# Kernel optimization log

Hardware: AMD Instinct MI355X
Metric: run time of the kernel (lower is better)

The kernel has to match this reference:

```python
import jax, jax.numpy as jnp
import numpy as np

B, T, OBS, ENC, H, A = 32, 512, 256, 1024, 1024, 64
AR_COEF, TAR_COEF = 0.01, 0.01
LN_EPS = 1e-5


def setup_inputs() -> dict:
    key = jax.random.key(0)
    ks = jax.random.split(key, 8)
    s = 0.02  # weight scale to keep activations in a sane range
    # PyTorch LSTM bias init in source: zeros, forget-gate slice [H:2H] = 1.0 (both b_ih and b_hh)
    b_gate = jnp.zeros((4 * H,), jnp.float32).at[H:2 * H].set(1.0)
    return {
        "obs": jax.random.normal(ks[0], (B, T, OBS), jnp.float32),
        "hxs": jnp.zeros((B, H), jnp.float32),
        "cxs": jnp.zeros((B, H), jnp.float32),
        "W1": jax.random.normal(ks[1], (ENC, OBS), jnp.float32) * s,
        "b1": jnp.zeros((ENC,), jnp.float32),
        "W2": jax.random.normal(ks[2], (ENC, ENC), jnp.float32) * s,
        "b2": jnp.zeros((ENC,), jnp.float32),
        "W_ih": jax.random.normal(ks[3], (4 * H, ENC), jnp.float32) * s,
        "W_hh": jax.random.normal(ks[4], (4 * H, H), jnp.float32) * s,
        "b_ih": b_gate,
        "b_hh": b_gate,
        "ln_g": jnp.ones((H,), jnp.float32),
        "ln_b": jnp.zeros((H,), jnp.float32),
        "Wa": jax.random.normal(ks[5], (A, H), jnp.float32) * s,
        "ba": jnp.zeros((A,), jnp.float32),
        "Wc": jax.random.normal(ks[6], (1, H), jnp.float32) * s,
        "bc": jnp.zeros((1,), jnp.float32),
    }


def reference(obs, hxs, cxs, W1, b1, W2, b2, W_ih, W_hh, b_ih, b_hh,
              ln_g, ln_b, Wa, ba, Wc, bc):
    # Encoder: Linear -> SiLU -> Linear -> SiLU
    enc = jax.nn.silu(obs @ W1.T + b1)
    enc = jax.nn.silu(enc @ W2.T + b2)  # (B,T,ENC)

    # LSTM (WeightDrop is identity in eval mode / p=0). Precompute input gates.
    gx = enc @ W_ih.T + (b_ih + b_hh)  # (B,T,4H)

    def step(carry, g_t):
        h, c = carry
        g = g_t + h @ W_hh.T  # (B,4H), PyTorch gate order: i, f, g, o
        i, f, gc, o = jnp.split(g, 4, axis=-1)
        c = jax.nn.sigmoid(f) * c + jax.nn.sigmoid(i) * jnp.tanh(gc)
        h = jax.nn.sigmoid(o) * jnp.tanh(c)
        return (h, c), h

    (h_n, c_n), hs = jax.lax.scan(step, (hxs, cxs), jnp.swapaxes(gx, 0, 1))
    out = jnp.swapaxes(hs, 0, 1)  # (B,T,H)

    # LayerNorm
    mu = out.mean(-1, keepdims=True)
    var = out.var(-1, keepdims=True)
    out = (out - mu) / jnp.sqrt(var + LN_EPS) * ln_g + ln_b

    ar_loss = jnp.mean(out ** 2) * AR_COEF
    tar_loss = jnp.mean((out[:, 1:, :] - out[:, :-1, :]) ** 2) * TAR_COEF

    logits = out @ Wa.T + ba          # (B,T,A)
    values = (out @ Wc.T + bc)[..., 0]  # (B,T)
    return logits, values, h_n, c_n, ar_loss, tar_loss
```

## Files before the change

### kernel.cpp

```cpp
#include <hip/hip_runtime.h>


typedef _Float16 half8 __attribute__((ext_vector_type(8)));
typedef _Float16 half4v __attribute__((ext_vector_type(4)));
typedef float floatx4 __attribute__((ext_vector_type(4)));
typedef unsigned long long ull;

__device__ __forceinline__ float sigmoidf_(float x) { return 1.f / (1.f + __expf(-x)); }

__global__ void k_convert(const float* __restrict__ src, _Float16* __restrict__ dst, int n4) {
  int i = blockIdx.x * blockDim.x + threadIdx.x;
  int stride = gridDim.x * blockDim.x;
  for (; i < n4; i += stride) {
    floatx4 v = *(const floatx4*)(src + (size_t)i * 4);
    half4v h;
    h[0] = (_Float16)v[0]; h[1] = (_Float16)v[1];
    h[2] = (_Float16)v[2]; h[3] = (_Float16)v[3];
    *(half4v*)(dst + (size_t)i * 4) = h;
  }
}

__global__ __launch_bounds__(256) void k_inith(const float* __restrict__ hxs,
                                               _Float16* __restrict__ hstate) {
  int s = blockIdx.x * 256 + threadIdx.x;
  int batch = s >> 9, pair = s & 511;
  union { _Float16 h[2]; unsigned u; } p;
  p.h[0] = (_Float16)hxs[batch * 1024 + pair * 2];
  p.h[1] = (_Float16)hxs[batch * 1024 + pair * 2 + 1];
  *(unsigned*)(hstate + (size_t)batch * 1024 + pair * 2) = p.u;
}

template<int EPI>
__global__ __launch_bounds__(256) void k_gemm(
    const _Float16* __restrict__ A, const _Float16* __restrict__ B,
    _Float16* __restrict__ C, const float* __restrict__ bias0,
    const float* __restrict__ bias1, int M, int N, int K)
{
  __shared__ _Float16 As[128 * 32];
  __shared__ _Float16 Bs[128 * 32];
  const int tid = threadIdx.x;
  const int l = tid & 63;
  const int w = tid >> 6;
  const int wr = w >> 1, wc = w & 1;
  const _Float16* Ab = A + (size_t)blockIdx.x * 128 * K;
  const _Float16* Bb = B + (size_t)blockIdx.y * 128 * K;

  floatx4 acc[4][4];
#pragma unroll
  for (int a = 0; a < 4; ++a)
#pragma unroll
    for (int b = 0; b < 4; ++b) acc[a][b] = (floatx4){0.f, 0.f, 0.f, 0.f};

  const int ci0 = tid, ci1 = tid + 256;
  const int r0 = ci0 >> 2, r1 = ci1 >> 2;
  const int q0 = (ci0 & 3) ^ ((r0 >> 2) & 3);
  const int q1 = (ci1 & 3) ^ ((r1 >> 2) & 3);
  const int lr = l & 15;
  const int ko = l >> 4;
  const int nkt = K >> 5;

  for (int kt = 0; kt < nkt; ++kt) {
    const _Float16* Ak = Ab + kt * 32;
    const _Float16* Bk = Bb + kt * 32;
    uint4 va0 = *(const uint4*)(Ak + (size_t)r0 * K + q0 * 8);
    uint4 va1 = *(const uint4*)(Ak + (size_t)r1 * K + q1 * 8);
    uint4 vb0 = *(const uint4*)(Bk + (size_t)r0 * K + q0 * 8);
    uint4 vb1 = *(const uint4*)(Bk + (size_t)r1 * K + q1 * 8);
    __syncthreads();
    *(uint4*)(As + ci0 * 8) = va0;
    *(uint4*)(As + ci1 * 8) = va1;
    *(uint4*)(Bs + ci0 * 8) = vb0;
    *(uint4*)(Bs + ci1 * 8) = vb1;
    __syncthreads();
    half8 af[4], bf[4];
#pragma unroll
    for (int mr = 0; mr < 4; ++mr) {
      int row = wr * 64 + mr * 16 + lr;
      int cq = ko ^ ((row >> 2) & 3);
      af[mr] = *(const half8*)(As + row * 32 + cq * 8);
    }
#pragma unroll
    for (int nc = 0; nc < 4; ++nc) {
      int col = wc * 64 + nc * 16 + lr;
      int cq = ko ^ ((col >> 2) & 3);
      bf[nc] = *(const half8*)(Bs + col * 32 + cq * 8);
    }
#pragma unroll
    for (int mr = 0; mr < 4; ++mr)
#pragma unroll
      for (int nc = 0; nc < 4; ++nc)
        acc[mr][nc] = __builtin_amdgcn_mfma_f32_16x16x32_f16(af[mr], bf[nc], acc[mr][nc], 0, 0, 0);
  }

  const int lq = l >> 4;
#pragma unroll
  for (int nc = 0; nc < 4; ++nc) {
    int gcol = blockIdx.y * 128 + wc * 64 + nc * 16 + lr;
    float bia = bias0[gcol];
    if (EPI == 1) bia += bias1[gcol];
#pragma unroll
    for (int mr = 0; mr < 4; ++mr) {
      int grow = blockIdx.x * 128 + wr * 64 + mr * 16 + lq * 4;
#pragma unroll
      for (int i = 0; i < 4; ++i) {
        float v = acc[mr][nc][i] + bia;
        if (EPI == 0) v = v * sigmoidf_(v);
        C[(size_t)(grow + i) * N + gcol] = (_Float16)v;
      }
    }
  }
}

__global__ __launch_bounds__(256, 1) void k_scan(
    const _Float16* __restrict__ gx,
    const _Float16* __restrict__ Whh,
    const float* __restrict__ cxs,
    _Float16* __restrict__ hstate,
    int* __restrict__ flags,
    _Float16* __restrict__ outh,
    float* __restrict__ out_hn, float* __restrict__ out_cn)
{
  const int blk = blockIdx.x;
  const int hbase = blk * 16;
  const int tid = threadIdx.x, l = tid & 63, wq = tid >> 6;
  __shared__ float red[4][4][2][4][65];

  const int cc = l & 15, ko = l >> 4;

  half8 bfr[4][8];
#pragma unroll
  for (int q = 0; q < 4; ++q)
#pragma unroll
    for (int kk = 0; kk < 8; ++kk)
      bfr[q][kk] = *(const half8*)(Whh + (size_t)(q * 1024 + hbase + cc) * 1024
                                   + wq * 256 + kk * 32 + ko * 8);

  const int gb = tid >> 3, gc2 = tid & 7;
  float c0 = cxs[gb * 1024 + hbase + gc2 * 2 + 0];
  float c1 = cxs[gb * 1024 + hbase + gc2 * 2 + 1];
  const int gmt = gb >> 4, greg = gb & 3;
  const int lane0 = ((gb & 15) >> 2) * 16 + gc2 * 2;

  unsigned gxv[4];
#pragma unroll
  for (int q = 0; q < 4; ++q)
    gxv[q] = *(const unsigned*)(gx + (size_t)gb * 512 * 4096
                                + q * 1024 + hbase + gc2 * 2);

  for (int t = 0; t < 512; ++t) {
    if (t > 0) {
      if (wq == 0) {
        const int* fp = flags + l * 16;
        int guard = 0;
        while (__hip_atomic_load(fp, __ATOMIC_RELAXED, __HIP_MEMORY_SCOPE_AGENT) < t) {
          if (++guard > (1 << 17)) break;
          __builtin_amdgcn_s_sleep(1);
        }
      }
      __builtin_amdgcn_s_barrier();
      __builtin_amdgcn_sched_barrier(0);
    }

    const _Float16* hcur = hstate + (size_t)(t & 1) * 32768;
    const ull* p0 = (const ull*)(hcur + cc * 1024 + wq * 256 + ko * 8);
    const ull* p1 = (const ull*)(hcur + (16 + cc) * 1024 + wq * 256 + ko * 8);
    ull ld0[16], ld1[16];
#pragma unroll
    for (int kk = 0; kk < 8; ++kk) {
      ld0[kk * 2 + 0] = __hip_atomic_load(p0 + kk * 8 + 0, __ATOMIC_RELAXED, __HIP_MEMORY_SCOPE_AGENT);
      ld0[kk * 2 + 1] = __hip_atomic_load(p0 + kk * 8 + 1, __ATOMIC_RELAXED, __HIP_MEMORY_SCOPE_AGENT);
      ld1[kk * 2 + 0] = __hip_atomic_load(p1 + kk * 8 + 0, __ATOMIC_RELAXED, __HIP_MEMORY_SCOPE_AGENT);
      ld1[kk * 2 + 1] = __hip_atomic_load(p1 + kk * 8 + 1, __ATOMIC_RELAXED, __HIP_MEMORY_SCOPE_AGENT);
    }

    floatx4 acc[4][2];
#pragma unroll
    for (int q = 0; q < 4; ++q) {
      acc[q][0] = (floatx4){0.f, 0.f, 0.f, 0.f};
      acc[q][1] = (floatx4){0.f, 0.f, 0.f, 0.f};
    }
#pragma unroll
    for (int kk = 0; kk < 8; ++kk) {
      union { ull u2[2]; half8 h; } a0, a1;
      a0.u2[0] = ld0[kk * 2 + 0]; a0.u2[1] = ld0[kk * 2 + 1];
      a1.u2[0] = ld1[kk * 2 + 0]; a1.u2[1] = ld1[kk * 2 + 1];
#pragma unroll
      for (int q = 0; q < 4; ++q) {
        acc[q][0] = __builtin_amdgcn_mfma_f32_16x16x32_f16(a0.h, bfr[q][kk], acc[q][0], 0, 0, 0);
        acc[q][1] = __builtin_amdgcn_mfma_f32_16x16x32_f16(a1.h, bfr[q][kk], acc[q][1], 0, 0, 0);
      }
    }
#pragma unroll
    for (int q = 0; q < 4; ++q)
#pragma unroll
      for (int mt = 0; mt < 2; ++mt)
#pragma unroll
        for (int i = 0; i < 4; ++i)
          red[wq][q][mt][i][l] = acc[q][mt][i];
    asm volatile("s_waitcnt lgkmcnt(0)" ::: "memory");
    __builtin_amdgcn_s_barrier();
    __builtin_amdgcn_sched_barrier(0);

    float pre0[4], pre1[4];
#pragma unroll
    for (int q = 0; q < 4; ++q) {
      pre0[q] = red[0][q][gmt][greg][lane0] + red[1][q][gmt][greg][lane0]
              + red[2][q][gmt][greg][lane0] + red[3][q][gmt][greg][lane0];
      pre1[q] = red[0][q][gmt][greg][lane0 + 1] + red[1][q][gmt][greg][lane0 + 1]
              + red[2][q][gmt][greg][lane0 + 1] + red[3][q][gmt][greg][lane0 + 1];
    }
    union { unsigned u; _Float16 h[2]; } g0, g1, g2, g3;
    g0.u = gxv[0]; g1.u = gxv[1]; g2.u = gxv[2]; g3.u = gxv[3];

    float i0 = sigmoidf_(pre0[0] + (float)g0.h[0]);
    float f0 = sigmoidf_(pre0[1] + (float)g1.h[0]);
    float gg0 = tanhf(pre0[2] + (float)g2.h[0]);
    float o0 = sigmoidf_(pre0[3] + (float)g3.h[0]);
    c0 = f0 * c0 + i0 * gg0;
    float h0 = o0 * tanhf(c0);

    float i1 = sigmoidf_(pre1[0] + (float)g0.h[1]);
    float f1 = sigmoidf_(pre1[1] + (float)g1.h[1]);
    float gg1 = tanhf(pre1[2] + (float)g2.h[1]);
    float o1 = sigmoidf_(pre1[3] + (float)g3.h[1]);
    c1 = f1 * c1 + i1 * gg1;
    float h1 = o1 * tanhf(c1);

    union { _Float16 h[2]; unsigned u; } hp;
    hp.h[0] = (_Float16)h0; hp.h[1] = (_Float16)h1;

    __hip_atomic_store((unsigned*)(hstate + (size_t)((t + 1) & 1) * 32768
                                   + (size_t)gb * 1024 + hbase + gc2 * 2),
                       hp.u, __ATOMIC_RELAXED, __HIP_MEMORY_SCOPE_AGENT);
    *(unsigned*)(outh + ((size_t)gb * 512 + t) * 1024 + hbase + gc2 * 2) = hp.u;
    if (t == 511) {
      float2 hv; hv.x = h0; hv.y = h1;
      float2 cv; cv.x = c0; cv.y = c1;
      *(float2*)(out_hn + gb * 1024 + hbase + gc2 * 2) = hv;
      *(float2*)(out_cn + gb * 1024 + hbase + gc2 * 2) = cv;
    }

    if (t < 511) {
#pragma unroll
      for (int q = 0; q < 4; ++q)
        gxv[q] = *(const unsigned*)(gx + ((size_t)gb * 512 + t + 1) * 4096
                                    + q * 1024 + hbase + gc2 * 2);
    }

    asm volatile("s_waitcnt vmcnt(0)" ::: "memory");
    __builtin_amdgcn_sched_barrier(0);
    __builtin_amdgcn_s_barrier();
    if (tid == 0 && t < 511)
      __hip_atomic_store(flags + blk * 16, t + 1, __ATOMIC_RELAXED,
                         __HIP_MEMORY_SCOPE_AGENT);
  }
}

__global__ __launch_bounds__(256) void k_ln(
    const _Float16* __restrict__ x, const float* __restrict__ gam,
    const float* __restrict__ bet, _Float16* __restrict__ y,
    float* __restrict__ arpart)
{
  const int m = blockIdx.x;
  const int tid = threadIdx.x;
  const int w = tid >> 6, l = tid & 63;
  half4v v = *(const half4v*)(x + (size_t)m * 1024 + tid * 4);
  float xv[4]; float s = 0.f, ss = 0.f;
#pragma unroll
  for (int j = 0; j < 4; ++j) { xv[j] = (float)v[j]; s += xv[j]; ss += xv[j] * xv[j]; }
#pragma unroll
  for (int off = 32; off > 0; off >>= 1) { s += __shfl_xor(s, off, 64); ss += __shfl_xor(ss, off, 64); }
  __shared__ float sw[4], ssw[4], bcast[2];
  if (l == 0) { sw[w] = s; ssw[w] = ss; }
  __syncthreads();
  if (tid == 0) {
    float S = sw[0] + sw[1] + sw[2] + sw[3];
    float SS = ssw[0] + ssw[1] + ssw[2] + ssw[3];
    float mu = S * (1.f / 1024.f);
    float var = SS * (1.f / 1024.f) - mu * mu;
    bcast[0] = mu; bcast[1] = rsqrtf(var + 1e-5f);
  }
  __syncthreads();
  float mu = bcast[0], rstd = bcast[1];
  float part = 0.f; half4v o;
#pragma unroll
  for (int j = 0; j < 4; ++j) {
    float nv = (xv[j] - mu) * rstd * gam[tid * 4 + j] + bet[tid * 4 + j];
    o[j] = (_Float16)nv;
    part += nv * nv;
  }
  *(half4v*)(y + (size_t)m * 1024 + tid * 4) = o;
#pragma unroll
  for (int off = 32; off > 0; off >>= 1) part += __shfl_xor(part, off, 64);
  if (l == 0) sw[w] = part;
  __syncthreads();
  if (tid == 0) arpart[m] = sw[0] + sw[1] + sw[2] + sw[3];
}

__global__ __launch_bounds__(256) void k_tar(const _Float16* __restrict__ y, float* __restrict__ tarpart) {
  const int tid = threadIdx.x;
  int gid = blockIdx.x * 256 + tid;
  const int stride = gridDim.x * 256;
  const int TOT = 32 * 511 * 256;
  float s = 0.f;
  for (int v = gid; v < TOT; v += stride) {
    int b = v / (511 * 256);
    int r = v - b * (511 * 256);
    size_t base = (size_t)b * 512 * 1024 + (size_t)r * 4;
    half4v a = *(const half4v*)(y + base);
    half4v c = *(const half4v*)(y + base + 1024);
#pragma unroll
    for (int j = 0; j < 4; ++j) { float d = (float)c[j] - (float)a[j]; s += d * d; }
  }
#pragma unroll
  for (int off = 32; off > 0; off >>= 1) s += __shfl_xor(s, off, 64);
  __shared__ float sw[4];
  if ((tid & 63) == 0) sw[tid >> 6] = s;
  __syncthreads();
  if (tid == 0) tarpart[blockIdx.x] = sw[0] + sw[1] + sw[2] + sw[3];
}

__global__ __launch_bounds__(256) void k_reduce(
    const float* __restrict__ arpart, const float* __restrict__ tarpart,
    float* __restrict__ dst)
{
  const int tid = threadIdx.x;
  float a = 0.f, t = 0.f;
  for (int i = tid; i < 16384; i += 256) a += arpart[i];
  for (int i = tid; i < 2048; i += 256) t += tarpart[i];
#pragma unroll
  for (int off = 32; off > 0; off >>= 1) { a += __shfl_xor(a, off, 64); t += __shfl_xor(t, off, 64); }
  __shared__ float sa[4], st[4];
  if ((tid & 63) == 0) { sa[tid >> 6] = a; st[tid >> 6] = t; }
  __syncthreads();
  if (tid == 0) {
    dst[0] = (sa[0] + sa[1] + sa[2] + sa[3]) * (0.01f / 16777216.f);
    dst[1] = (st[0] + st[1] + st[2] + st[3]) * (0.01f / 16744448.f);
  }
}

__global__ __launch_bounds__(256) void k_logits(
    const _Float16* __restrict__ X, const _Float16* __restrict__ Wa,
    const float* __restrict__ ba, float* __restrict__ out)
{
  const int tid = threadIdx.x, l = tid & 63, w = tid >> 6;
  const int lr = l & 15, lq = l >> 4;
  const int rowb = blockIdx.x * 64 + w * 16;
  floatx4 acc[4];
#pragma unroll
  for (int nc = 0; nc < 4; ++nc) acc[nc] = (floatx4){0.f, 0.f, 0.f, 0.f};
  for (int kc = 0; kc < 32; ++kc) {
    int k = kc * 32 + lq * 8;
    half8 af = *(const half8*)(X + (size_t)(rowb + lr) * 1024 + k);
#pragma unroll
    for (int nc = 0; nc < 4; ++nc) {
      half8 bf = *(const half8*)(Wa + (size_t)(nc * 16 + lr) * 1024 + k);
      acc[nc] = __builtin_amdgcn_mfma_f32_16x16x32_f16(af, bf, acc[nc], 0, 0, 0);
    }
  }
#pragma unroll
  for (int nc = 0; nc < 4; ++nc) {
    int col = nc * 16 + lr;
    float bia = ba[col];
#pragma unroll
    for (int i = 0; i < 4; ++i) {
      int grow = rowb + lq * 4 + i;
      out[(size_t)grow * 64 + col] = acc[nc][i] + bia;
    }
  }
}

__global__ __launch_bounds__(256) void k_values(
    const _Float16* __restrict__ X, const _Float16* __restrict__ Wc,
    const float* __restrict__ bc, float* __restrict__ out)
{
  const int tid = threadIdx.x, l = tid & 63, w = tid >> 6;
  half8 w0 = *(const half8*)(Wc + l * 16);
  half8 w1 = *(const half8*)(Wc + l * 16 + 8);
  float bias = bc[0];
  const int rowb = blockIdx.x * 64 + w * 16;
  for (int r = 0; r < 16; ++r) {
    const _Float16* xr = X + (size_t)(rowb + r) * 1024 + l * 16;
    half8 x0 = *(const half8*)(xr);
    half8 x1 = *(const half8*)(xr + 8);
    float s = 0.f;
#pragma unroll
    for (int j = 0; j < 8; ++j) s += (float)x0[j] * (float)w0[j] + (float)x1[j] * (float)w1[j];
#pragma unroll
    for (int off = 32; off > 0; off >>= 1) s += __shfl_xor(s, off, 64);
    if (l == 0) out[rowb + r] = s + bias;
  }
}

extern "C" void kernel_launch(void* const* d_in, const int* in_sizes, int n_in,
                              void* d_out, int out_size, void* d_ws, size_t ws_size,
                              hipStream_t stream)
{
  const float* obs = (const float*)d_in[0];
  const float* hxs = (const float*)d_in[1];
  const float* cxs = (const float*)d_in[2];
  const float* W1  = (const float*)d_in[3];
  const float* b1  = (const float*)d_in[4];
  const float* W2  = (const float*)d_in[5];
  const float* b2  = (const float*)d_in[6];
  const float* Wih = (const float*)d_in[7];
  const float* Whh = (const float*)d_in[8];
  const float* bih = (const float*)d_in[9];
  const float* bhh = (const float*)d_in[10];
  const float* lng = (const float*)d_in[11];
  const float* lnb = (const float*)d_in[12];
  const float* Wa  = (const float*)d_in[13];
  const float* ba  = (const float*)d_in[14];
  const float* Wc  = (const float*)d_in[15];
  const float* bc  = (const float*)d_in[16];

  char* ws = (char*)d_ws;
  size_t off = 0;
  auto alloc = [&](size_t bytes) -> char* {
    char* p = ws + off;
    off += (bytes + 255) & ~(size_t)255;
    return p;
  };
  _Float16* obs16 = (_Float16*)alloc(4194304ull * 2);
  _Float16* W1x   = (_Float16*)alloc(262144ull * 2);
  _Float16* W2x   = (_Float16*)alloc(1048576ull * 2);
  _Float16* Wihx  = (_Float16*)alloc(4194304ull * 2);
  _Float16* Whhx  = (_Float16*)alloc(4194304ull * 2);
  _Float16* Wax   = (_Float16*)alloc(65536ull * 2);
  _Float16* Wcx   = (_Float16*)alloc(1024ull * 2);
  _Float16* enc1  = (_Float16*)alloc(16384ull * 1024 * 2);
  _Float16* enc2  = (_Float16*)alloc(16384ull * 1024 * 2);
  _Float16* gx    = (_Float16*)alloc(16384ull * 4096 * 2);
  _Float16* hstate= (_Float16*)alloc(2ull * 32 * 1024 * 2);
  int* flags      = (int*)alloc(64ull * 16 * 4);
  _Float16* outh  = (_Float16*)alloc(16384ull * 1024 * 2);
  float* arpart   = (float*)alloc(16384ull * 4);
  float* tarpart  = (float*)alloc(2048ull * 4);
  _Float16* normed = enc1;

  float* out_f      = (float*)d_out;
  float* out_logits = out_f;
  float* out_values = out_f + 1048576;
  float* out_hn     = out_f + 1064960;
  float* out_cn     = out_f + 1097728;
  float* out_loss   = out_f + 1130496;

  hipMemsetAsync(flags, 0, 64ull * 16 * 4, stream);
  k_inith<<<64, 256, 0, stream>>>(hxs, hstate);

  auto conv = [&](const float* s, _Float16* d, int n) {
    int n4 = n >> 2;
    int grid = (n4 + 255) / 256;
    if (grid > 2048) grid = 2048;
    k_convert<<<grid, 256, 0, stream>>>(s, d, n4);
  };
  conv(obs, obs16, 4194304);
  conv(W1, W1x, 262144);
  conv(W2, W2x, 1048576);
  conv(Wih, Wihx, 4194304);
  conv(Whh, Whhx, 4194304);
  conv(Wa, Wax, 65536);
  conv(Wc, Wcx, 1024);

  k_gemm<0><<<dim3(128, 8), 256, 0, stream>>>(obs16, W1x, enc1, b1, nullptr, 16384, 1024, 256);
  k_gemm<0><<<dim3(128, 8), 256, 0, stream>>>(enc1, W2x, enc2, b2, nullptr, 16384, 1024, 1024);
  k_gemm<1><<<dim3(128, 32), 256, 0, stream>>>(enc2, Wihx, gx, bih, bhh, 16384, 4096, 1024);
  k_scan<<<64, 256, 0, stream>>>(gx, Whhx, cxs, hstate, flags, outh, out_hn, out_cn);
  k_ln<<<16384, 256, 0, stream>>>(outh, lng, lnb, normed, arpart);
  k_tar<<<2048, 256, 0, stream>>>(normed, tarpart);
  k_reduce<<<1, 256, 0, stream>>>(arpart, tarpart, out_loss);
  k_logits<<<256, 256, 0, stream>>>(normed, Wax, ba, out_logits);
  k_values<<<256, 256, 0, stream>>>(normed, Wcx, bc, out_values);
  (void)in_sizes; (void)n_in; (void)out_size; (void)ws_size;
}
```

Before: 3.636 ms.

## Trim LSTM scan step latency and merge conversion launches

Four changes to shorten each step of the serial LSTM scan and cut launch overhead. In the scan, every wave now polls the per-block flags with a wave-wide __all vote instead of one wave polling and then hitting a block barrier. The flag publish is moved ahead of the outh and gx stores and loads, so the next step's dependency is released sooner. tanhf is replaced by a clamped exp-based approximation. All fp32-to-fp16 conversions, including the initial hidden state, are merged into one launch. The risks are higher polling pressure on the flags and a slight accuracy change from the fast tanh.

After: 3.342 ms (median of 3 runs). 8.1% less time.

```diff
diff --git a/kernel.cpp b/kernel.cpp
--- a/kernel.cpp
+++ b/kernel.cpp
@@ -7,27 +7,41 @@
 typedef unsigned long long ull;
 
 __device__ __forceinline__ float sigmoidf_(float x) { return 1.f / (1.f + __expf(-x)); }
-
-__global__ void k_convert(const float* __restrict__ src, _Float16* __restrict__ dst, int n4) {
-  int i = blockIdx.x * blockDim.x + threadIdx.x;
-  int stride = gridDim.x * blockDim.x;
-  for (; i < n4; i += stride) {
-    floatx4 v = *(const floatx4*)(src + (size_t)i * 4);
-    half4v h;
-    h[0] = (_Float16)v[0]; h[1] = (_Float16)v[1];
-    h[2] = (_Float16)v[2]; h[3] = (_Float16)v[3];
-    *(half4v*)(dst + (size_t)i * 4) = h;
-  }
-}
-
-__global__ __launch_bounds__(256) void k_inith(const float* __restrict__ hxs,
-                                               _Float16* __restrict__ hstate) {
-  int s = blockIdx.x * 256 + threadIdx.x;
-  int batch = s >> 9, pair = s & 511;
-  union { _Float16 h[2]; unsigned u; } p;
-  p.h[0] = (_Float16)hxs[batch * 1024 + pair * 2];
-  p.h[1] = (_Float16)hxs[batch * 1024 + pair * 2 + 1];
-  *(unsigned*)(hstate + (size_t)batch * 1024 + pair * 2) = p.u;
+__device__ __forceinline__ float tanhf_(float x) {
+  x = fminf(15.f, fmaxf(-15.f, x));
+  float e = __expf(-2.f * x);
+  return (1.f - e) / (1.f + e);
+}
+
+__global__ __launch_bounds__(256) void k_convert_all(
+    const float* s0, _Float16* d0, int n0,
+    const float* s1, _Float16* d1, int n1,
+    const float* s2, _Float16* d2, int n2,
+    const float* s3, _Float16* d3, int n3,
+    const float* s4, _Float16* d4, int n4,
+    const float* s5, _Float16* d5, int n5,
+    const float* s6, _Float16* d6, int n6,
+    const float* s7, _Float16* d7, int n7)
+{
+  const int gid = blockIdx.x * 256 + threadIdx.x;
+  const int stride = gridDim.x * 256;
+#define CONV_SEG(s, d, n)                                                  \
+  for (int i = gid; i < (n); i += stride) {                                \
+    floatx4 v = *(const floatx4*)((s) + (size_t)i * 4);                    \
+    half4v h;                                                              \
+    h[0] = (_Float16)v[0]; h[1] = (_Float16)v[1];                          \
+    h[2] = (_Float16)v[2]; h[3] = (_Float16)v[3];                          \
+    *(half4v*)((d) + (size_t)i * 4) = h;                                   \
+  }
+  CONV_SEG(s0, d0, n0)
+  CONV_SEG(s1, d1, n1)
+  CONV_SEG(s2, d2, n2)
+  CONV_SEG(s3, d3, n3)
+  CONV_SEG(s4, d4, n4)
+  CONV_SEG(s5, d5, n5)
+  CONV_SEG(s6, d6, n6)
+  CONV_SEG(s7, d7, n7)
+#undef CONV_SEG
 }
 
 template<int EPI>
@@ -149,15 +163,15 @@
 
   for (int t = 0; t < 512; ++t) {
     if (t > 0) {
-      if (wq == 0) {
-        const int* fp = flags + l * 16;
-        int guard = 0;
-        while (__hip_atomic_load(fp, __ATOMIC_RELAXED, __HIP_MEMORY_SCOPE_AGENT) < t) {
-          if (++guard > (1 << 17)) break;
-          __builtin_amdgcn_s_sleep(1);
-        }
+      const int* fp = flags + l * 16;
+      int guard = 0;
+      while (true) {
+        int f = __hip_atomic_load(fp, __ATOMIC_RELAXED, __HIP_MEMORY_SCOPE_AGENT);
+        if (__all(f >= t)) break;
+        if (++guard > (1 << 17)) break;
+        __builtin_amdgcn_s_sleep(1);
       }
-      __builtin_amdgcn_s_barrier();
+      asm volatile("" ::: "memory");
       __builtin_amdgcn_sched_barrier(0);
     }
 
@@ -214,17 +228,17 @@
 
     float i0 = sigmoidf_(pre0[0] + (float)g0.h[0]);
     float f0 = sigmoidf_(pre0[1] + (float)g1.h[0]);
-    float gg0 = tanhf(pre0[2] + (float)g2.h[0]);
+    float gg0 = tanhf_(pre0[2] + (float)g2.h[0]);
     float o0 = sigmoidf_(pre0[3] + (float)g3.h[0]);
     c0 = f0 * c0 + i0 * gg0;
-    float h0 = o0 * tanhf(c0);
+    float h0 = o0 * tanhf_(c0);
 
     float i1 = sigmoidf_(pre1[0] + (float)g0.h[1]);
     float f1 = sigmoidf_(pre1[1] + (float)g1.h[1]);
-    float gg1 = tanhf(pre1[2] + (float)g2.h[1]);
+    float gg1 = tanhf_(pre1[2] + (float)g2.h[1]);
     float o1 = sigmoidf_(pre1[3] + (float)g3.h[1]);
     c1 = f1 * c1 + i1 * gg1;
-    float h1 = o1 * tanhf(c1);
+    float h1 = o1 * tanhf_(c1);
 
     union { _Float16 h[2]; unsigned u; } hp;
     hp.h[0] = (_Float16)h0; hp.h[1] = (_Float16)h1;
@@ -232,27 +246,26 @@
     __hip_atomic_store((unsigned*)(hstate + (size_t)((t + 1) & 1) * 32768
                                    + (size_t)gb * 1024 + hbase + gc2 * 2),
                        hp.u, __ATOMIC_RELAXED, __HIP_MEMORY_SCOPE_AGENT);
+    asm volatile("s_waitcnt vmcnt(0)" ::: "memory");
+    __builtin_amdgcn_sched_barrier(0);
+    __builtin_amdgcn_s_barrier();
+    if (tid == 0 && t < 511)
+      __hip_atomic_store(flags + blk * 16, t + 1, __ATOMIC_RELAXED,
+                         __HIP_MEMORY_SCOPE_AGENT);
+
     *(unsigned*)(outh + ((size_t)gb * 512 + t) * 1024 + hbase + gc2 * 2) = hp.u;
     if (t == 511) {
       float2 hv; hv.x = h0; hv.y = h1;
       float2 cv; cv.x = c0; cv.y = c1;
       *(float2*)(out_hn + gb * 1024 + hbase + gc2 * 2) = hv;
       *(float2*)(out_cn + gb * 1024 + hbase + gc2 * 2) = cv;
-    }
-
-    if (t < 511) {
+    } else {
 #pragma unroll
       for (int q = 0; q < 4; ++q)
         gxv[q] = *(const unsigned*)(gx + ((size_t)gb * 512 + t + 1) * 4096
                                     + q * 1024 + hbase + gc2 * 2);
     }
-
-    asm volatile("s_waitcnt vmcnt(0)" ::: "memory");
     __builtin_amdgcn_sched_barrier(0);
-    __builtin_amdgcn_s_barrier();
-    if (tid == 0 && t < 511)
-      __hip_atomic_store(flags + blk * 16, t + 1, __ATOMIC_RELAXED,
-                         __HIP_MEMORY_SCOPE_AGENT);
   }
 }
 
@@ -446,21 +459,16 @@
   float* out_loss   = out_f + 1130496;
 
   hipMemsetAsync(flags, 0, 64ull * 16 * 4, stream);
-  k_inith<<<64, 256, 0, stream>>>(hxs, hstate);
-
-  auto conv = [&](const float* s, _Float16* d, int n) {
-    int n4 = n >> 2;
-    int grid = (n4 + 255) / 256;
-    if (grid > 2048) grid = 2048;
-    k_convert<<<grid, 256, 0, stream>>>(s, d, n4);
-  };
-  conv(obs, obs16, 4194304);
-  conv(W1, W1x, 262144);
-  conv(W2, W2x, 1048576);
-  conv(Wih, Wihx, 4194304);
-  conv(Whh, Whhx, 4194304);
-  conv(Wa, Wax, 65536);
-  conv(Wc, Wcx, 1024);
+
+  k_convert_all<<<2048, 256, 0, stream>>>(
+      obs, obs16, 4194304 / 4,
+      W1, W1x, 262144 / 4,
+      W2, W2x, 1048576 / 4,
+      Wih, Wihx, 4194304 / 4,
+      Whh, Whhx, 4194304 / 4,
+      Wa, Wax, 65536 / 4,
+      Wc, Wcx, 1024 / 4,
+      hxs, hstate, 32768 / 4);
 
   k_gemm<0><<<dim3(128, 8), 256, 0, stream>>>(obs16, W1x, enc1, b1, nullptr, 16384, 1024, 256);
   k_gemm<0><<<dim3(128, 8), 256, 0, stream>>>(enc1, W2x, enc2, b2, nullptr, 16384, 1024, 1024);
```
